# Kernel tuning notes

Measured on AMD Instinct MI355X. Metric: run time of the kernel, lower is better.

## Reference

```python
import jax, jax.numpy as jnp
import numpy as np

B, L, N, C = 4, 96, 200, 1
D, H, DH, M = 128, 8, 16, 16
DFF, E, TOPK, LAYERS = 512, 4, 2, 3
PRED, TOD = 96, 288
EPS = 1e-5


def layernorm(x, g, b):
    m = jnp.mean(x, -1, keepdims=True)
    v = jnp.mean((x - m) ** 2, -1, keepdims=True)
    return (x - m) / jnp.sqrt(v + EPS) * g + b


def performer(x, Wq, bq, Wk, bk, Wv, bv, Wo, bo, proj):
    # x: [..., S, D]; FAVOR+ softmax-kernel linear attention (non-causal)
    sh = x.shape
    def heads(t):
        return jnp.swapaxes(t.reshape(sh[:-1] + (H, DH)), -2, -3)  # [..., H, S, DH]
    q = heads(x @ Wq + bq)
    k = heads(x @ Wk + bk)
    v = heads(x @ Wv + bv)
    dn = DH ** -0.25
    q = q * dn
    k = k * dn
    qd = q @ proj  # [..., H, S, M]
    kd = k @ proj
    qn = 0.5 * jnp.sum(q * q, -1, keepdims=True)
    kn = 0.5 * jnp.sum(k * k, -1, keepdims=True)
    qp = jnp.exp(qd - qn - jnp.max(qd, -1, keepdims=True)) * (M ** -0.5) + 1e-6
    kp = jnp.exp(kd - kn - jnp.max(kd, axis=(-1, -2), keepdims=True)) * (M ** -0.5) + 1e-6
    kv = jnp.einsum('...lm,...ld->...md', kp, v)          # [..., H, M, DH]
    z = 1.0 / (jnp.einsum('...lm,...m->...l', qp, jnp.sum(kp, -2)) + 1e-6)
    o = jnp.einsum('...lm,...md->...ld', qp, kv) * z[..., None]
    o = jnp.swapaxes(o, -2, -3).reshape(sh)
    return o @ Wo + bo


def moe(x, Wg, W1, b1, W2, b2):
    # top-2 softmax gate with renormalized weights; experts are Linear-ReLU-Linear
    probs = jax.nn.softmax(x @ Wg, -1)
    tv, ti = jax.lax.top_k(probs, TOPK)
    w = tv / jnp.sum(tv, -1, keepdims=True)
    g = jnp.sum(jax.nn.one_hot(ti, E, dtype=x.dtype) * w[..., None], -2)  # [..., E]
    h = jax.nn.relu(jnp.einsum('...d,edf->...ef', x, W1) + b1)
    y = jnp.einsum('...ef,efd->...ed', h, W2) + b2
    return jnp.einsum('...ed,...e->...d', y, g)


def block(x, Wq, bq, Wk, bk, Wv, bv, Wo, bo, proj, Wg, W1, b1, W2, b2, g2, be2, g3, be3):
    a = performer(x, Wq, bq, Wk, bk, Wv, bv, Wo, bo, proj)
    x = layernorm(x + a, g2, be2)
    f = moe(x, Wg, W1, b1, W2, b2)
    return layernorm(x + f, g3, be3)


def _forward(x_enc, x_mark, emb_W, emb_b, tod_table, dow_table, adaptive_table, sp_W,
             sp_Wq, sp_bq, sp_Wk, sp_bk, sp_Wv, sp_bv, sp_Wo, sp_bo, sp_proj,
             sp_gate, sp_W1, sp_b1, sp_W2, sp_b2, sp_ln2_g, sp_ln2_b, sp_ln3_g, sp_ln3_b,
             proj_W, proj_b, LWq, Lbq, LWk, Lbk, LWv, Lbv, LWo, Lbo, Lproj,
             Lgate, LW1, Lb1, LW2, Lb2, Lln2g, Lln2b, Lln3g, Lln3b, mix_W, mix_b):
    # RevIN normalize (affine=False): stats over all dims except batch and last
    mean = jnp.mean(x_enc, axis=(1, 2), keepdims=True)
    std = jnp.sqrt(jnp.var(x_enc, axis=(1, 2), keepdims=True) + EPS)
    xn = (x_enc - mean) / std  # [B, L, N, C]
    # series decomposition, kernel=3, zero padding (count_include_pad)
    xp = jnp.pad(xn, ((0, 0), (1, 1), (0, 0), (0, 0)))
    trend = (xp[:, :-2] + xp[:, 1:-1] + xp[:, 2:]) / 3.0
    season = xn - trend
    # spatial embedding: [B,L,N,C] -> [B,N,L*C] -> [B,N,1,D] -> transformer block
    sp = jnp.swapaxes(xn, 1, 2).reshape(B, N, L * C) @ sp_W
    sp = block(sp[:, :, None, :], sp_Wq, sp_bq, sp_Wk, sp_bk, sp_Wv, sp_bv, sp_Wo, sp_bo,
               sp_proj, sp_gate, sp_W1, sp_b1, sp_W2, sp_b2, sp_ln2_g, sp_ln2_b, sp_ln3_g, sp_ln3_b)
    # trend / season embeddings with tod (col 6) and dow (col 2) mark features
    tod_f = jnp.broadcast_to(x_mark[:, :, None, 6:7], (B, L, N, 1))
    dow_f = jnp.broadcast_to(x_mark[:, :, None, 2:3], (B, L, N, 1))
    te = jnp.swapaxes(jnp.concatenate([trend, tod_f, dow_f], -1) @ emb_W + emb_b, 1, 2)  # [B,N,L,D]
    se = jnp.swapaxes(jnp.concatenate([season, tod_f, dow_f], -1) @ emb_W + emb_b, 1, 2)
    ad = jnp.broadcast_to(adaptive_table.reshape(1, N, L, D), (B, N, L, D))
    tod_idx = (x_mark[..., 6] * TOD).astype(jnp.int32)  # [B, L]
    tod_e = jnp.broadcast_to(tod_table[tod_idx][:, None], (B, N, L, D))
    dow_idx = x_mark[..., 2].astype(jnp.int32)
    dow_e = jnp.broadcast_to(dow_table[dow_idx][:, None], (B, N, L, D))
    spb = jnp.broadcast_to(sp, (B, N, L, D))
    xe = jnp.concatenate([te, se, ad, tod_e, dow_e, spb], -1) @ proj_W + proj_b  # [B,N,L,D]
    for i in range(LAYERS):
        xe = block(xe, LWq[i], Lbq[i], LWk[i], Lbk[i], LWv[i], Lbv[i], LWo[i], Lbo[i],
                   Lproj[i], Lgate[i], LW1[i], Lb1[i], LW2[i], Lb2[i],
                   Lln2g[i], Lln2b[i], Lln3g[i], Lln3b[i])
    out = xe.reshape(B, N, L * D) @ mix_W + mix_b  # [B, N, PRED*C]
    out = jnp.swapaxes(out.reshape(B, N, PRED, C), 1, 2)  # [B, PRED, N, C]
    return out * std + mean  # RevIN denorm


def setup_inputs() -> dict:
    key = jax.random.key(0)
    ks = iter(jax.random.split(key, 80))
    def nrm(shape, s=0.02):
        return jax.random.normal(next(ks), shape, jnp.float32) * s
    z = lambda shape: jnp.zeros(shape, jnp.float32)
    o = lambda shape: jnp.ones(shape, jnp.float32)
    d = {}
    d['x_enc'] = jax.random.normal(next(ks), (B, L, N, C), jnp.float32)
    xm = jax.random.uniform(next(ks), (B, L, 7), dtype=jnp.float32, minval=0.0, maxval=0.999)
    xm = xm.at[..., 2].set(jax.random.randint(next(ks), (B, L), 0, 7).astype(jnp.float32))
    d['x_mark'] = xm
    d['emb_W'] = nrm((C + 2, D)); d['emb_b'] = z((D,))
    d['tod_table'] = nrm((TOD, D)); d['dow_table'] = nrm((7, D))
    d['adaptive_table'] = nrm((L * N, D))
    d['sp_W'] = nrm((L * C, D))
    for nm in ['sp_Wq', 'sp_Wk', 'sp_Wv', 'sp_Wo']:
        d[nm] = nrm((D, D))
    for nm in ['sp_bq', 'sp_bk', 'sp_bv', 'sp_bo']:
        d[nm] = z((D,))
    d['sp_proj'] = jax.random.normal(next(ks), (DH, M), jnp.float32)
    d['sp_gate'] = nrm((D, E))
    d['sp_W1'] = nrm((E, D, DFF)); d['sp_b1'] = z((E, DFF))
    d['sp_W2'] = nrm((E, DFF, D)); d['sp_b2'] = z((E, D))
    d['sp_ln2_g'] = o((D,)); d['sp_ln2_b'] = z((D,))
    d['sp_ln3_g'] = o((D,)); d['sp_ln3_b'] = z((D,))
    d['proj_W'] = nrm((6 * D, D)); d['proj_b'] = z((D,))
    for nm in ['LWq', 'LWk', 'LWv', 'LWo']:
        d[nm] = nrm((LAYERS, D, D))
    for nm in ['Lbq', 'Lbk', 'Lbv', 'Lbo']:
        d[nm] = z((LAYERS, D))
    d['Lproj'] = jax.random.normal(next(ks), (LAYERS, DH, M), jnp.float32)
    d['Lgate'] = nrm((LAYERS, D, E))
    d['LW1'] = nrm((LAYERS, E, D, DFF)); d['Lb1'] = z((LAYERS, E, DFF))
    d['LW2'] = nrm((LAYERS, E, DFF, D)); d['Lb2'] = z((LAYERS, E, D))
    d['Lln2g'] = o((LAYERS, D)); d['Lln2b'] = z((LAYERS, D))
    d['Lln3g'] = o((LAYERS, D)); d['Lln3b'] = z((LAYERS, D))
    d['mix_W'] = nrm((L * D, PRED * C)); d['mix_b'] = z((PRED * C,))
    return d


def reference(x_enc, x_mark, emb_W, emb_b, tod_table, dow_table, adaptive_table, sp_W,
              sp_Wq, sp_bq, sp_Wk, sp_bk, sp_Wv, sp_bv, sp_Wo, sp_bo, sp_proj,
              sp_gate, sp_W1, sp_b1, sp_W2, sp_b2, sp_ln2_g, sp_ln2_b, sp_ln3_g, sp_ln3_b,
              proj_W, proj_b, LWq, Lbq, LWk, Lbk, LWv, Lbv, LWo, Lbo, Lproj,
              Lgate, LW1, Lb1, LW2, Lb2, Lln2g, Lln2b, Lln3g, Lln3b, mix_W, mix_b):
    return _forward(x_enc, x_mark, emb_W, emb_b, tod_table, dow_table, adaptive_table, sp_W,
                    sp_Wq, sp_bq, sp_Wk, sp_bk, sp_Wv, sp_bv, sp_Wo, sp_bo, sp_proj,
                    sp_gate, sp_W1, sp_b1, sp_W2, sp_b2, sp_ln2_g, sp_ln2_b, sp_ln3_g, sp_ln3_b,
                    proj_W, proj_b, LWq, Lbq, LWk, Lbk, LWv, Lbv, LWo, Lbo, Lproj,
                    Lgate, LW1, Lb1, LW2, Lb2, Lln2g, Lln2b, Lln3g, Lln3b, mix_W, mix_b)
```

## Files before the change

### kernel.cpp

```cpp
#include <hip/hip_runtime.h>
#include <stdint.h>

typedef unsigned short u16;
typedef __attribute__((ext_vector_type(8))) __bf16 bf16x8;
typedef __attribute__((ext_vector_type(4))) float f32x4;

#define Bb 4
#define Ll 96
#define Nn 200
#define Dd 128
#define Hh 8
#define Tt 76800
#define RSEQ 800
#define PREDp 96

__device__ __forceinline__ u16 f2b(float f) {
  union { float f; uint32_t u; } c; c.f = f;
  return (u16)((c.u + 0x7FFFu + ((c.u >> 16) & 1u)) >> 16);
}
__device__ __forceinline__ float b2f(u16 h) {
  union { uint32_t u; float f; } c; c.u = ((uint32_t)h) << 16;
  return c.f;
}

#define LDKV 72

template<int MODE, int DUAL, int AF32>
__global__ __launch_bounds__(256) void gemm_bf16(
    const u16* __restrict__ A, size_t aPl, const u16* __restrict__ Bt, size_t bPl,
    const float* __restrict__ bias, float* Cf, u16* Cb, size_t cPl,
    int R, int K, int N, int kchunk,
    const float* __restrict__ G, int expert, int accum)
{
  __shared__ u16 As[128 * LDKV];
  __shared__ u16 Bs[128 * LDKV];
  __shared__ u16 Asl[DUAL ? 128 * LDKV : 2];
  __shared__ u16 Bsl[DUAL ? 128 * LDKV : 2];
  const int tid = threadIdx.x;
  const int bM = blockIdx.x * 128, bN = blockIdx.y * 128;
  const int klo = blockIdx.z * kchunk;
  const int khi = (K < klo + kchunk) ? K : (klo + kchunk);
  const int wave = tid >> 6, lane = tid & 63;
  const int wr = (wave >> 1) * 64, wc = (wave & 1) * 64;
  const int lr = lane & 15, kg = (lane >> 4) * 8;
  f32x4 acc[4][4];
  const f32x4 zz = {0.f, 0.f, 0.f, 0.f};
#pragma unroll
  for (int m = 0; m < 4; m++)
#pragma unroll
    for (int n = 0; n < 4; n++) acc[m][n] = zz;

  for (int k0 = klo; k0 < khi; k0 += 64) {
#pragma unroll
    for (int i = 0; i < 4; i++) {
      int v = tid + i * 256;
      int r = v >> 3, c8 = (v & 7) * 8;
      int gr = bM + r, gc = bN + r;
      bool aok = gr < R;
      if (AF32) {
        const float* Af = (const float*)A;
        float4 f0 = make_float4(0, 0, 0, 0), f1 = make_float4(0, 0, 0, 0);
        if (aok) {
          f0 = *(const float4*)(Af + (size_t)gr * K + k0 + c8);
          f1 = *(const float4*)(Af + (size_t)gr * K + k0 + c8 + 4);
        }
        float ff[8] = {f0.x, f0.y, f0.z, f0.w, f1.x, f1.y, f1.z, f1.w};
        union { int4 v4; u16 us[8]; } hu, lu;
#pragma unroll
        for (int j = 0; j < 8; j++) {
          u16 h = f2b(ff[j]);
          hu.us[j] = h;
          lu.us[j] = f2b(ff[j] - b2f(h));
        }
        *(int4*)(&As[r * LDKV + c8]) = hu.v4;
        *(int4*)(&Asl[r * LDKV + c8]) = lu.v4;
      } else {
        int4 av = make_int4(0, 0, 0, 0);
        if (aok) av = *(const int4*)(A + (size_t)gr * K + k0 + c8);
        *(int4*)(&As[r * LDKV + c8]) = av;
        if (DUAL) {
          int4 av2 = make_int4(0, 0, 0, 0);
          if (aok) av2 = *(const int4*)(A + aPl + (size_t)gr * K + k0 + c8);
          *(int4*)(&Asl[r * LDKV + c8]) = av2;
        }
      }
      int4 bv = make_int4(0, 0, 0, 0);
      if (gc < N) bv = *(const int4*)(Bt + (size_t)gc * K + k0 + c8);
      *(int4*)(&Bs[r * LDKV + c8]) = bv;
      if (DUAL) {
        int4 bv2 = make_int4(0, 0, 0, 0);
        if (gc < N) bv2 = *(const int4*)(Bt + bPl + (size_t)gc * K + k0 + c8);
        *(int4*)(&Bsl[r * LDKV + c8]) = bv2;
      }
    }
    __syncthreads();
#pragma unroll
    for (int kk = 0; kk < 64; kk += 32) {
      bf16x8 ah[4], bh[4], al[4], bl[4];
#pragma unroll
      for (int m = 0; m < 4; m++) ah[m] = *(const bf16x8*)(&As[(wr + m * 16 + lr) * LDKV + kk + kg]);
#pragma unroll
      for (int n = 0; n < 4; n++) bh[n] = *(const bf16x8*)(&Bs[(wc + n * 16 + lr) * LDKV + kk + kg]);
      if (DUAL) {
#pragma unroll
        for (int m = 0; m < 4; m++) al[m] = *(const bf16x8*)(&Asl[(wr + m * 16 + lr) * LDKV + kk + kg]);
#pragma unroll
        for (int n = 0; n < 4; n++) bl[n] = *(const bf16x8*)(&Bsl[(wc + n * 16 + lr) * LDKV + kk + kg]);
      }
#pragma unroll
      for (int m = 0; m < 4; m++)
#pragma unroll
        for (int n = 0; n < 4; n++) {
          acc[m][n] = __builtin_amdgcn_mfma_f32_16x16x32_bf16(ah[m], bh[n], acc[m][n], 0, 0, 0);
          if (DUAL) {
            acc[m][n] = __builtin_amdgcn_mfma_f32_16x16x32_bf16(ah[m], bl[n], acc[m][n], 0, 0, 0);
            acc[m][n] = __builtin_amdgcn_mfma_f32_16x16x32_bf16(al[m], bh[n], acc[m][n], 0, 0, 0);
          }
        }
    }
    __syncthreads();
  }

  const int row0 = bM + wr + (lane >> 4) * 4;
  const int col0 = bN + wc + (lane & 15);
#pragma unroll
  for (int m = 0; m < 4; m++) {
#pragma unroll
    for (int n = 0; n < 4; n++) {
      int col = col0 + n * 16;
      if (col >= N) continue;
#pragma unroll
      for (int r = 0; r < 4; r++) {
        int row = row0 + m * 16 + r;
        if (row >= R) continue;
        float v = acc[m][n][r];
        size_t ci = (size_t)row * N + col;
        if (MODE == 3) {
          atomicAdd(Cf + ci, v);
        } else {
          if (bias) v += bias[col];
          if (MODE == 1) v = fmaxf(v, 0.f);
          if (MODE == 2) {
            v *= G[row * 4 + expert];
            if (accum) v += Cf[ci];
            Cf[ci] = v;
          } else {
            if (Cf) Cf[ci] = v;
            if (Cb) {
              u16 h = f2b(v);
              Cb[ci] = h;
              if (cPl) Cb[cPl + ci] = f2b(v - b2f(h));
            }
          }
        }
      }
    }
  }
}

#define LDH 520
__global__ __launch_bounds__(256) void moe_ffn(
    const u16* __restrict__ X2B, const u16* __restrict__ W1T, const u16* __restrict__ W2T,
    const float* __restrict__ b1, const float* __restrict__ b2,
    const float* __restrict__ G, const int* __restrict__ midx, const int* __restrict__ mcnt,
    const int* __restrict__ js, float* __restrict__ Yc)
{
  __shared__ u16 As[32 * 136];
  __shared__ u16 Ws[128 * 136];
  __shared__ u16 Hs[32 * LDH];
  __shared__ int tok_l[32];
  __shared__ int js_l[32];
  __shared__ float gt_l[32];
  const int e = blockIdx.y;
  const int cnt = mcnt[e];
  const int t0 = blockIdx.x * 32;
  if (t0 >= cnt) return;
  const int tid = threadIdx.x;
  const int wave = tid >> 6, lane = tid & 63;
  const int mw = wave >> 1, nw = wave & 1;
  const int lr = lane & 15, kg = (lane >> 4) * 8;
  const int rowq = (lane >> 4) * 4;
  if (tid < 32) {
    int slot = t0 + tid;
    int tk = (slot < cnt) ? midx[e * Tt + slot] : -1;
    tok_l[tid] = tk;
    js_l[tid] = (slot < cnt) ? js[e * Tt + slot] : 0;
    gt_l[tid] = (tk >= 0) ? G[(size_t)tk * 4 + e] : 0.f;
  }
  __syncthreads();
  {
    int v = tid;
#pragma unroll
    for (int i = 0; i < 2; i++, v += 256) {
      int r = v >> 4, c8 = (v & 15) * 8;
      int tk = tok_l[r];
      int4 av = make_int4(0, 0, 0, 0);
      if (tk >= 0) av = *(const int4*)(X2B + (size_t)tk * 128 + c8);
      *(int4*)(&As[r * 136 + c8]) = av;
    }
  }
  const u16* W1e = W1T + (size_t)e * 512 * 128;
  const u16* W2e = W2T + (size_t)e * 128 * 512;
  for (int ns = 0; ns < 4; ns++) {
    __syncthreads();
    {
      int v = tid;
#pragma unroll
      for (int i = 0; i < 8; i++, v += 256) {
        int r = v >> 4, c8 = (v & 15) * 8;
        *(int4*)(&Ws[r * 136 + c8]) = *(const int4*)(W1e + (size_t)(ns * 128 + r) * 128 + c8);
      }
    }
    __syncthreads();
    f32x4 acc[4];
    const f32x4 zz = {0.f, 0.f, 0.f, 0.f};
#pragma unroll
    for (int n = 0; n < 4; n++) acc[n] = zz;
#pragma unroll
    for (int kk = 0; kk < 128; kk += 32) {
      bf16x8 a = *(const bf16x8*)(&As[(mw * 16 + lr) * 136 + kk + kg]);
#pragma unroll
      for (int n = 0; n < 4; n++) {
        bf16x8 b = *(const bf16x8*)(&Ws[(nw * 64 + n * 16 + lr) * 136 + kk + kg]);
        acc[n] = __builtin_amdgcn_mfma_f32_16x16x32_bf16(a, b, acc[n], 0, 0, 0);
      }
    }
#pragma unroll
    for (int n = 0; n < 4; n++) {
#pragma unroll
      for (int r = 0; r < 4; r++) {
        int row = mw * 16 + rowq + r;
        int colh = ns * 128 + nw * 64 + n * 16 + lr;
        float hv = fmaxf(acc[n][r] + b1[e * 512 + colh], 0.f);
        Hs[row * LDH + (colh ^ ((row & 7) << 3))] = f2b(hv);
      }
    }
  }
  f32x4 acc2[4];
  const f32x4 zz2 = {0.f, 0.f, 0.f, 0.f};
#pragma unroll
  for (int n = 0; n < 4; n++) acc2[n] = zz2;
  for (int ks = 0; ks < 4; ks++) {
    __syncthreads();
    {
      int v = tid;
#pragma unroll
      for (int i = 0; i < 8; i++, v += 256) {
        int r = v >> 4, c8 = (v & 15) * 8;
        *(int4*)(&Ws[r * 136 + c8]) = *(const int4*)(W2e + (size_t)r * 512 + ks * 128 + c8);
      }
    }
    __syncthreads();
#pragma unroll
    for (int kk = 0; kk < 128; kk += 32) {
      int row = mw * 16 + lr;
      int k = ks * 128 + kk + kg;
      bf16x8 a = *(const bf16x8*)(&Hs[row * LDH + (k ^ ((row & 7) << 3))]);
#pragma unroll
      for (int n = 0; n < 4; n++) {
        bf16x8 b = *(const bf16x8*)(&Ws[(nw * 64 + n * 16 + lr) * 136 + kk + kg]);
        acc2[n] = __builtin_amdgcn_mfma_f32_16x16x32_bf16(a, b, acc2[n], 0, 0, 0);
      }
    }
  }
#pragma unroll
  for (int n = 0; n < 4; n++) {
#pragma unroll
    for (int r = 0; r < 4; r++) {
      int rloc = mw * 16 + rowq + r;
      if (t0 + rloc >= cnt) continue;
      int col = nw * 64 + n * 16 + lr;
      float v = (acc2[n][r] + b2[e * 128 + col]) * gt_l[rloc];
      Yc[(size_t)js_l[rloc] * 128 + col] = v;
    }
  }
}

__global__ void moe_combine(const float4* __restrict__ Yc, float4* __restrict__ Rb, int n4) {
  int i = blockIdx.x * 256 + threadIdx.x;
  if (i >= n4) return;
  int t = i >> 5, c = i & 31;
  float4 a = Yc[(size_t)t * 64 + c];
  float4 b = Yc[(size_t)t * 64 + 32 + c];
  float4 o; o.x = a.x + b.x; o.y = a.y + b.y; o.z = a.z + b.z; o.w = a.w + b.w;
  Rb[i] = o;
}

__global__ void prep_wt_tiled(const float* __restrict__ W, u16* __restrict__ Wt,
                              int K, int N, int KP, int NP, size_t PL, size_t bstride)
{
  __shared__ float tile[32][33];
  int k0 = blockIdx.x * 32, n0 = blockIdx.y * 32;
  int bb = blockIdx.z;
  const float* Wb = W + (size_t)bb * K * N;
  u16* Wtb = Wt + (size_t)bb * bstride;
  for (int i = threadIdx.y; i < 32; i += 8) {
    int k = k0 + i, n = n0 + threadIdx.x;
    tile[i][threadIdx.x] = (k < K && n < N) ? Wb[(size_t)k * N + n] : 0.f;
  }
  __syncthreads();
  for (int i = threadIdx.y; i < 32; i += 8) {
    int n = n0 + i, k = k0 + threadIdx.x;
    if (n < NP && k < KP) {
      float v = tile[threadIdx.x][i];
      u16 h = f2b(v);
      Wtb[(size_t)n * KP + k] = h;
      if (PL) Wtb[PL + (size_t)n * KP + k] = f2b(v - b2f(h));
    }
  }
}

__global__ void copy_dual(const float* __restrict__ s, u16* __restrict__ d, int n, size_t PL) {
  int i = blockIdx.x * 256 + threadIdx.x;
  if (i < n) {
    float v = s[i];
    u16 h = f2b(v);
    d[i] = h;
    d[PL + i] = f2b(v - b2f(h));
  }
}
__global__ void zero_f32(float* p, int n) {
  int i = blockIdx.x * 256 + threadIdx.x;
  if (i < n) p[i] = 0.f;
}

__global__ __launch_bounds__(256) void revin_stats(const float* __restrict__ x, float* stats) {
  int b = blockIdx.x;
  __shared__ float ss[256], sq[256];
  float s = 0.f, q = 0.f;
  for (int i = threadIdx.x; i < Ll * Nn; i += 256) {
    float v = x[(size_t)b * Ll * Nn + i];
    s += v; q += v * v;
  }
  ss[threadIdx.x] = s; sq[threadIdx.x] = q;
  __syncthreads();
  for (int st = 128; st > 0; st >>= 1) {
    if (threadIdx.x < st) { ss[threadIdx.x] += ss[threadIdx.x + st]; sq[threadIdx.x] += sq[threadIdx.x + st]; }
    __syncthreads();
  }
  if (threadIdx.x == 0) {
    float mean = ss[0] / (float)(Ll * Nn);
    float var = sq[0] / (float)(Ll * Nn) - mean * mean;
    float sd = sqrtf(var + 1e-5f);
    stats[b] = mean; stats[4 + b] = 1.f / sd; stats[8 + b] = sd;
  }
}

__global__ void calc_vecs(const float* __restrict__ embW, const float* __restrict__ embB,
                          const float* __restrict__ projW, const float* __restrict__ projB,
                          float* __restrict__ vecs)
{
  int j = threadIdx.x;
  float a = 0, b = 0, c = 0, d = 0, e = 0;
  for (int k = 0; k < 128; k++) {
    float p0 = projW[(size_t)k * 128 + j];
    float p1 = projW[(size_t)(128 + k) * 128 + j];
    a += embW[k] * p0;
    b += embW[k] * p1;
    c += embW[128 + k] * (p0 + p1);
    d += embW[256 + k] * (p0 + p1);
    e += embB[k] * (p0 + p1);
  }
  vecs[j] = a; vecs[128 + j] = b; vecs[256 + j] = c; vecs[384 + j] = d;
  vecs[512 + j] = e + projB[j];
}

__global__ void concat_qkvb(const float* __restrict__ bq, const float* __restrict__ bk,
                            const float* __restrict__ bv, float* __restrict__ out)
{
  int t = blockIdx.x * 128 + threadIdx.x;
  if (t >= 3 * 384) return;
  int layer = t / 384, r = t % 384, part = r / 128, col = r % 128;
  const float* src = part == 0 ? bq : (part == 1 ? bk : bv);
  out[t] = src[layer * 128 + col];
}

__global__ void xs_build(const float* __restrict__ x, const float* __restrict__ stats,
                         u16* __restrict__ xs, size_t PL)
{
  int r = blockIdx.x;
  int l = threadIdx.x;
  int b = r / Nn, n = r % Nn;
  float v = 0.f;
  if (l < Ll) v = (x[((size_t)(b * Ll + l) * Nn + n)] - stats[b]) * stats[4 + b];
  u16 h = f2b(v);
  xs[(size_t)r * 128 + l] = h;
  xs[PL + (size_t)r * 128 + l] = f2b(v - b2f(h));
}

__global__ __launch_bounds__(128) void sp_perf(const float* __restrict__ qf, const float* __restrict__ kf,
                                               const float* __restrict__ vf, const float* __restrict__ proj,
                                               u16* __restrict__ ob, size_t PL)
{
  int r = blockIdx.x, tid = threadIdx.x;
  __shared__ float ql[128], kl[128], vl[128], ps[256];
  ql[tid] = qf[(size_t)r * 128 + tid] * 0.5f;
  kl[tid] = kf[(size_t)r * 128 + tid] * 0.5f;
  vl[tid] = vf[(size_t)r * 128 + tid];
  ps[tid] = proj[tid]; ps[128 + tid] = proj[128 + tid];
  __syncthreads();
  int h = tid >> 4, m = tid & 15;
  float qd = 0, kd = 0, qn = 0, kn = 0;
#pragma unroll
  for (int d = 0; d < 16; d++) {
    float qv = ql[h * 16 + d], kv_ = kl[h * 16 + d];
    qd += qv * ps[d * 16 + m]; kd += kv_ * ps[d * 16 + m];
    qn += qv * qv; kn += kv_ * kv_;
  }
  qn *= 0.5f; kn *= 0.5f;
  float qmax = qd, kmax = kd;
  for (int msk = 8; msk; msk >>= 1) {
    qmax = fmaxf(qmax, __shfl_xor(qmax, msk, 16));
    kmax = fmaxf(kmax, __shfl_xor(kmax, msk, 16));
  }
  float qp = expf(qd - qn - qmax) * 0.25f + 1e-6f;
  float kp = expf(kd - kn - kmax) * 0.25f + 1e-6f;
  float t = qp * kp;
  for (int msk = 8; msk; msk >>= 1) t += __shfl_xor(t, msk, 16);
  float f = t / (t + 1e-6f);
  float o = vl[tid] * f;
  u16 hh = f2b(o);
  ob[(size_t)r * 128 + tid] = hh;
  ob[PL + (size_t)r * 128 + tid] = f2b(o - b2f(hh));
}

__global__ __launch_bounds__(256) void performer_attn2(
    const float* __restrict__ qkv, const float* __restrict__ proj, float* __restrict__ ao)
{
  __shared__ float ks[2][96 * 17];
  __shared__ float vs[2][96 * 17];
  __shared__ float kvs[2][16 * 17];
  __shared__ float ksum[2][16];
  __shared__ float red[2][96];
  __shared__ float ps[256];
  const int tid = threadIdx.x;
  const int seq = blockIdx.x >> 2, hp = blockIdx.x & 3;
  ps[tid] = proj[tid];
#pragma unroll
  for (int i = 0; i < 3; i++) {
    int idx = tid + i * 256;
    int row = idx >> 3, c4 = idx & 7;
    int hl = c4 >> 2, d0 = (c4 & 3) * 4;
    size_t gb = ((size_t)seq * 96 + row) * 384 + hp * 32 + hl * 16 + d0;
    float4 k4 = *(const float4*)(qkv + gb + 128);
    float4 v4 = *(const float4*)(qkv + gb + 256);
    int lb = row * 17 + d0;
    ks[hl][lb + 0] = k4.x * 0.5f; ks[hl][lb + 1] = k4.y * 0.5f;
    ks[hl][lb + 2] = k4.z * 0.5f; ks[hl][lb + 3] = k4.w * 0.5f;
    vs[hl][lb + 0] = v4.x; vs[hl][lb + 1] = v4.y;
    vs[hl][lb + 2] = v4.z; vs[hl][lb + 3] = v4.w;
  }
  const int h = tid / 96, s = tid - h * 96;
  float q[16];
  if (tid < 192) {
    size_t qb_ = ((size_t)seq * 96 + s) * 384 + hp * 32 + h * 16;
#pragma unroll
    for (int i = 0; i < 4; i++) {
      float4 t = *(const float4*)(qkv + qb_ + i * 4);
      q[i * 4] = t.x * 0.5f; q[i * 4 + 1] = t.y * 0.5f;
      q[i * 4 + 2] = t.z * 0.5f; q[i * 4 + 3] = t.w * 0.5f;
    }
  }
  __syncthreads();
  float qd[16], kd[16], qp[16];
  float qn = 0.f, kn = 0.f;
  if (tid < 192) {
#pragma unroll
    for (int d = 0; d < 16; d++) {
      float kv = ks[h][s * 17 + d];
      qn += q[d] * q[d]; kn += kv * kv;
    }
    qn *= 0.5f; kn *= 0.5f;
#pragma unroll
    for (int m = 0; m < 16; m++) {
      float aq = 0.f, ak = 0.f;
#pragma unroll
      for (int d = 0; d < 16; d++) {
        aq += q[d] * ps[d * 16 + m];
        ak += ks[h][s * 17 + d] * ps[d * 16 + m];
      }
      qd[m] = aq; kd[m] = ak;
    }
    float km = kd[0];
#pragma unroll
    for (int m = 1; m < 16; m++) km = fmaxf(km, kd[m]);
    red[h][s] = km;
  }
  __syncthreads();
  if (tid < 192 && s < 48) red[h][s] = fmaxf(red[h][s], red[h][s + 48]);
  __syncthreads();
  if (tid < 192 && s < 24) red[h][s] = fmaxf(red[h][s], red[h][s + 24]);
  __syncthreads();
  if (tid < 192 && s < 12) red[h][s] = fmaxf(red[h][s], red[h][s + 12]);
  __syncthreads();
  if (tid < 192 && s < 6) red[h][s] = fmaxf(red[h][s], red[h][s + 6]);
  __syncthreads();
  if (tid < 192 && s < 3) red[h][s] = fmaxf(red[h][s], red[h][s + 3]);
  __syncthreads();
  if (tid < 192) {
    float kmax = fmaxf(fmaxf(red[h][0], red[h][1]), red[h][2]);
    float qmx = qd[0];
#pragma unroll
    for (int m = 1; m < 16; m++) qmx = fmaxf(qmx, qd[m]);
#pragma unroll
    for (int m = 0; m < 16; m++) {
      qp[m] = expf(qd[m] - qn - qmx) * 0.25f + 1e-6f;
      ks[h][s * 17 + m] = expf(kd[m] - kn - kmax) * 0.25f + 1e-6f;
    }
  }
  __syncthreads();
#pragma unroll
  for (int it = 0; it < 2; it++) {
    int idx = tid + it * 256;
    int hh = idx >> 8, mm = (idx >> 4) & 15, dd = idx & 15;
    float a0 = 0.f, a1 = 0.f, a2 = 0.f, a3 = 0.f;
    for (int s2 = 0; s2 < 96; s2 += 4) {
      a0 += ks[hh][(s2 + 0) * 17 + mm] * vs[hh][(s2 + 0) * 17 + dd];
      a1 += ks[hh][(s2 + 1) * 17 + mm] * vs[hh][(s2 + 1) * 17 + dd];
      a2 += ks[hh][(s2 + 2) * 17 + mm] * vs[hh][(s2 + 2) * 17 + dd];
      a3 += ks[hh][(s2 + 3) * 17 + mm] * vs[hh][(s2 + 3) * 17 + dd];
    }
    kvs[hh][mm * 17 + dd] = (a0 + a1) + (a2 + a3);
  }
  if (tid < 32) {
    int hh = tid >> 4, mm = tid & 15;
    float a0 = 0.f, a1 = 0.f, a2 = 0.f, a3 = 0.f;
    for (int s2 = 0; s2 < 96; s2 += 4) {
      a0 += ks[hh][(s2 + 0) * 17 + mm];
      a1 += ks[hh][(s2 + 1) * 17 + mm];
      a2 += ks[hh][(s2 + 2) * 17 + mm];
      a3 += ks[hh][(s2 + 3) * 17 + mm];
    }
    ksum[hh][mm] = (a0 + a1) + (a2 + a3);
  }
  __syncthreads();
  if (tid < 192) {
    float zd = 1e-6f;
#pragma unroll
    for (int m = 0; m < 16; m++) zd += qp[m] * ksum[h][m];
    float zi = 1.f / zd;
#pragma unroll
    for (int d = 0; d < 16; d++) {
      float a = 0.f;
#pragma unroll
      for (int m = 0; m < 16; m++) a += qp[m] * kvs[h][m * 17 + d];
      ks[h][s * 17 + d] = a * zi;
    }
  }
  __syncthreads();
#pragma unroll
  for (int i = 0; i < 3; i++) {
    int idx = tid + i * 256;
    int row = idx >> 3, c4 = idx & 7;
    int hl = c4 >> 2, d0 = (c4 & 3) * 4;
    int lb = row * 17 + d0;
    float4 o;
    o.x = ks[hl][lb + 0]; o.y = ks[hl][lb + 1]; o.z = ks[hl][lb + 2]; o.w = ks[hl][lb + 3];
    *(float4*)(ao + ((size_t)seq * 96 + row) * 128 + hp * 32 + hl * 16 + d0) = o;
  }
}

__global__ __launch_bounds__(256) void ln_fused(const u16* __restrict__ Xin, size_t xPl,
    const float* __restrict__ Res,
    const float* __restrict__ g, const float* __restrict__ bta,
    u16* __restrict__ Out, size_t oPl, int R)
{
  int wave = threadIdx.x >> 6, lane = threadIdx.x & 63;
  int tok = blockIdx.x * 4 + wave;
  if (tok >= R) return;
  size_t bo = (size_t)tok * 128 + lane * 2;
  ushort2 h2 = *(const ushort2*)(Xin + bo);
  ushort2 l2 = *(const ushort2*)(Xin + xPl + bo);
  float2 rv = *(const float2*)(Res + bo);
  float a0 = b2f(h2.x) + b2f(l2.x) + rv.x;
  float a1 = b2f(h2.y) + b2f(l2.y) + rv.y;
  float s = a0 + a1, sq = a0 * a0 + a1 * a1;
  for (int m = 32; m; m >>= 1) { s += __shfl_xor(s, m); sq += __shfl_xor(sq, m); }
  float mean = s * (1.f / 128.f);
  float var = sq * (1.f / 128.f) - mean * mean;
  float rstd = rsqrtf(var + 1e-5f);
  float g0 = g[lane * 2], g1 = g[lane * 2 + 1], b0 = bta[lane * 2], b1 = bta[lane * 2 + 1];
  float o0 = (a0 - mean) * rstd * g0 + b0;
  float o1 = (a1 - mean) * rstd * g1 + b1;
  u16 u0 = f2b(o0), u1 = f2b(o1);
  ushort2 hh; hh.x = u0; hh.y = u1;
  ushort2 ll; ll.x = f2b(o0 - b2f(u0)); ll.y = f2b(o1 - b2f(u1));
  *(ushort2*)(Out + bo) = hh;
  *(ushort2*)(Out + oPl + bo) = ll;
}

__global__ __launch_bounds__(256) void gate_topk(const u16* __restrict__ X, size_t xPl,
    const float* __restrict__ Wg, float* __restrict__ Gout, int R)
{
  int gid = blockIdx.x * 256 + threadIdx.x;
  int tok = gid >> 2, sub = gid & 3;
  if (tok >= R) return;
  float pr0 = 0, pr1 = 0, pr2 = 0, pr3 = 0;
  for (int d0 = 0; d0 < 32; d0 += 8) {
    size_t idx = (size_t)tok * 128 + sub * 32 + d0;
    int4 hv = *(const int4*)(X + idx);
    int4 lv = *(const int4*)(X + xPl + idx);
    const u16* hp = (const u16*)&hv;
    const u16* lp = (const u16*)&lv;
#pragma unroll
    for (int j = 0; j < 8; j++) {
      float xj = b2f(hp[j]) + b2f(lp[j]);
      float4 w = *(const float4*)(Wg + (size_t)(sub * 32 + d0 + j) * 4);
      pr0 += xj * w.x; pr1 += xj * w.y; pr2 += xj * w.z; pr3 += xj * w.w;
    }
  }
  pr0 += __shfl_xor(pr0, 1, 4); pr0 += __shfl_xor(pr0, 2, 4);
  pr1 += __shfl_xor(pr1, 1, 4); pr1 += __shfl_xor(pr1, 2, 4);
  pr2 += __shfl_xor(pr2, 1, 4); pr2 += __shfl_xor(pr2, 2, 4);
  pr3 += __shfl_xor(pr3, 1, 4); pr3 += __shfl_xor(pr3, 2, 4);
  float mx = fmaxf(fmaxf(pr0, pr1), fmaxf(pr2, pr3));
  float e0 = expf(pr0 - mx), e1 = expf(pr1 - mx), e2 = expf(pr2 - mx), e3 = expf(pr3 - mx);
  int i1 = 0; float t1 = e0;
  if (e1 > t1) { t1 = e1; i1 = 1; }
  if (e2 > t1) { t1 = e2; i1 = 2; }
  if (e3 > t1) { t1 = e3; i1 = 3; }
  float t2 = -1.f; int i2 = 0;
  if (0 != i1 && e0 > t2) { t2 = e0; i2 = 0; }
  if (1 != i1 && e1 > t2) { t2 = e1; i2 = 1; }
  if (2 != i1 && e2 > t2) { t2 = e2; i2 = 2; }
  if (3 != i1 && e3 > t2) { t2 = e3; i2 = 3; }
  float own = (sub == 0) ? e0 : ((sub == 1) ? e1 : ((sub == 2) ? e2 : e3));
  float gv = (sub == i1 || sub == i2) ? own / (t1 + t2) : 0.f;
  Gout[(size_t)tok * 4 + sub] = gv;
}

__global__ void moe_zero_counts(int* counts) {
  if (threadIdx.x < 4) counts[threadIdx.x] = 0;
}
__global__ __launch_bounds__(256) void moe_fill(const float* __restrict__ G,
    int* __restrict__ counts, int* __restrict__ idx, int* __restrict__ js, int R)
{
  int tok = blockIdx.x * 256 + threadIdx.x;
  if (tok >= R) return;
  float4 g = *(const float4*)(G + (size_t)tok * 4);
  int j = 0;
  if (g.x > 0.f) { int p = atomicAdd(counts + 0, 1); idx[0 * Tt + p] = tok; js[0 * Tt + p] = tok * 2 + j; j++; }
  if (g.y > 0.f) { int p = atomicAdd(counts + 1, 1); idx[1 * Tt + p] = tok; js[1 * Tt + p] = tok * 2 + j; j++; }
  if (g.z > 0.f) { int p = atomicAdd(counts + 2, 1); idx[2 * Tt + p] = tok; js[2 * Tt + p] = tok * 2 + j; j++; }
  if (g.w > 0.f) { int p = atomicAdd(counts + 3, 1); idx[3 * Tt + p] = tok; js[3 * Tt + p] = tok * 2 + j; j++; }
}

__global__ __launch_bounds__(128) void embed_combine(
    const float* __restrict__ xenc, const float* __restrict__ xmark,
    const float* __restrict__ stats, const float* __restrict__ vecs,
    const float* __restrict__ adP, const float* __restrict__ ttP,
    const float* __restrict__ ddP, const float* __restrict__ spP,
    u16* __restrict__ XB, size_t PL)
{
  int t = blockIdx.x;
  int l = t % 96; int bn = t / 96; int n = bn % Nn; int b = bn / Nn;
  float mean = stats[b], rstd = stats[4 + b];
  float x0 = (xenc[((size_t)(b * Ll + l) * Nn + n)] - mean) * rstd;
  float xm = 0.f, xp = 0.f;
  if (l > 0)  xm = (xenc[((size_t)(b * Ll + l - 1) * Nn + n)] - mean) * rstd;
  if (l < 95) xp = (xenc[((size_t)(b * Ll + l + 1) * Nn + n)] - mean) * rstd;
  float trend = (xm + x0 + xp) * (1.f / 3.f);
  float season = x0 - trend;
  const float* mk = xmark + (size_t)(b * Ll + l) * 7;
  float todf = mk[6], dowf = mk[2];
  int ti = (int)(todf * 288.f);
  int di = (int)dowf;
  int j = threadIdx.x;
  float v = trend * vecs[j] + season * vecs[128 + j] + todf * vecs[256 + j] + dowf * vecs[384 + j]
          + vecs[512 + j]
          + adP[((size_t)n * 96 + l) * 128 + j]
          + ttP[(size_t)ti * 128 + j]
          + ddP[(size_t)di * 128 + j]
          + spP[(size_t)bn * 128 + j];
  u16 h = f2b(v);
  XB[(size_t)t * 128 + j] = h;
  XB[PL + (size_t)t * 128 + j] = f2b(v - b2f(h));
}

__global__ void final_out(const float* __restrict__ mixC, const float* __restrict__ mixb,
                          const float* __restrict__ stats, float* __restrict__ out)
{
  int i = blockIdx.x * 256 + threadIdx.x;
  if (i >= Bb * PREDp * Nn) return;
  int n = i % Nn; int p = (i / Nn) % PREDp; int b = i / (Nn * PREDp);
  out[i] = (mixC[((size_t)(b * Nn + n)) * PREDp + p] + mixb[p]) * stats[8 + b] + stats[b];
}

extern "C" void kernel_launch(void* const* d_in, const int* in_sizes, int n_in,
                              void* d_out, int out_size, void* d_ws, size_t ws_size,
                              hipStream_t stream)
{
  const float* x_enc   = (const float*)d_in[0];
  const float* x_mark  = (const float*)d_in[1];
  const float* emb_W   = (const float*)d_in[2];
  const float* emb_b   = (const float*)d_in[3];
  const float* tod_tab = (const float*)d_in[4];
  const float* dow_tab = (const float*)d_in[5];
  const float* adapt   = (const float*)d_in[6];
  const float* sp_W    = (const float*)d_in[7];
  const float* sp_Wq   = (const float*)d_in[8];
  const float* sp_Wk   = (const float*)d_in[9];
  const float* sp_Wv   = (const float*)d_in[10];
  const float* sp_Wo   = (const float*)d_in[11];
  const float* sp_bq   = (const float*)d_in[12];
  const float* sp_bk   = (const float*)d_in[13];
  const float* sp_bv   = (const float*)d_in[14];
  const float* sp_bo   = (const float*)d_in[15];
  const float* sp_proj = (const float*)d_in[16];
  const float* sp_gate = (const float*)d_in[17];
  const float* sp_W1   = (const float*)d_in[18];
  const float* sp_b1   = (const float*)d_in[19];
  const float* sp_W2   = (const float*)d_in[20];
  const float* sp_b2   = (const float*)d_in[21];
  const float* sp_l2g  = (const float*)d_in[22];
  const float* sp_l2b  = (const float*)d_in[23];
  const float* sp_l3g  = (const float*)d_in[24];
  const float* sp_l3b  = (const float*)d_in[25];
  const float* proj_W  = (const float*)d_in[26];
  const float* proj_b  = (const float*)d_in[27];
  const float* LWq     = (const float*)d_in[28];
  const float* LWk     = (const float*)d_in[29];
  const float* LWv     = (const float*)d_in[30];
  const float* LWo     = (const float*)d_in[31];
  const float* Lbq     = (const float*)d_in[32];
  const float* Lbk     = (const float*)d_in[33];
  const float* Lbv     = (const float*)d_in[34];
  const float* Lbo     = (const float*)d_in[35];
  const float* Lproj   = (const float*)d_in[36];
  const float* Lgate   = (const float*)d_in[37];
  const float* LW1     = (const float*)d_in[38];
  const float* Lb1     = (const float*)d_in[39];
  const float* LW2     = (const float*)d_in[40];
  const float* Lb2     = (const float*)d_in[41];
  const float* Ll2g    = (const float*)d_in[42];
  const float* Ll2b    = (const float*)d_in[43];
  const float* Ll3g    = (const float*)d_in[44];
  const float* Ll3b    = (const float*)d_in[45];
  const float* mix_W   = (const float*)d_in[46];
  const float* mix_b   = (const float*)d_in[47];

  if (n_in < 48) return;
  if (in_sizes[0] != Bb * Ll * Nn) return;
  if (in_sizes[26] != 768 * 128) return;
  if (in_sizes[38] != 3 * 4 * 128 * 512) return;
  if (in_sizes[46] != 12288 * 96) return;

  char* base = (char*)d_ws;
  size_t off = 0;
  auto alloc = [&](size_t bytes) -> char* {
    char* p = base + off;
    off += (bytes + 255) & ~(size_t)255;
    return p;
  };
  const size_t PT128 = (size_t)Tt * 128;
  const int CH = Tt / 2;

  float* stats = (float*)alloc(12 * 4);
  float* vecs  = (float*)alloc(5 * 128 * 4);
  float* mixC  = (float*)alloc((size_t)RSEQ * 96 * 4);
  float* Gt    = (float*)alloc((size_t)Tt * 4 * 4);
  float* Gsp   = (float*)alloc((size_t)RSEQ * 4 * 4);
  int* midx    = (int*)alloc((size_t)4 * Tt * 4);
  int* jsarr   = (int*)alloc((size_t)4 * Tt * 4);
  int* mcnt    = (int*)alloc(256);
  float* qkvb  = (float*)alloc((size_t)3 * 384 * 4);
  u16* XB    = (u16*)alloc(PT128 * 2 * 2);
  u16* X2B   = (u16*)alloc(PT128 * 2 * 2);
  float* Rb  = (float*)alloc(PT128 * 4);
  u16* spWt  = (u16*)alloc((size_t)128 * 128 * 2 * 2);
  u16* spWqT = (u16*)alloc((size_t)128 * 128 * 2 * 2);
  u16* spWkT = (u16*)alloc((size_t)128 * 128 * 2 * 2);
  u16* spWvT = (u16*)alloc((size_t)128 * 128 * 2 * 2);
  u16* spWoT = (u16*)alloc((size_t)128 * 128 * 2 * 2);
  u16* LWqkvT = (u16*)alloc((size_t)3 * 384 * 128 * 2 * 2);
  u16* LWoT  = (u16*)alloc((size_t)3 * 128 * 128 * 2 * 2);
  u16* spW1T = (u16*)alloc((size_t)4 * 512 * 128 * 2 * 2);
  u16* spW2T = (u16*)alloc((size_t)4 * 128 * 512 * 2 * 2);
  u16* LW1T  = (u16*)alloc((size_t)12 * 512 * 128 * 2);
  u16* LW2T  = (u16*)alloc((size_t)12 * 128 * 512 * 2);
  u16* PT    = (u16*)alloc((size_t)4 * 128 * 128 * 2 * 2);
  u16* mixWT = (u16*)alloc((size_t)96 * 12288 * 2 * 2);

  const size_t B3 = (size_t)Tt * 2 * 128 * 4;
  char* regB = alloc(B3);
  size_t boff = 0;
  auto balloc = [&](size_t bytes) -> char* {
    char* p = regB + boff;
    boff += (bytes + 255) & ~(size_t)255;
    return p;
  };
  float* adP   = (float*)balloc((size_t)19200 * 128 * 4);
  float* ttP   = (float*)balloc((size_t)288 * 128 * 4);
  float* ddP   = (float*)balloc((size_t)7 * 128 * 4);
  float* spP   = (float*)balloc((size_t)RSEQ * 128 * 4);
  u16* adb     = (u16*)balloc((size_t)19200 * 128 * 2 * 2);
  u16* ttb     = (u16*)balloc((size_t)288 * 128 * 2 * 2);
  u16* ddb     = (u16*)balloc((size_t)7 * 128 * 2 * 2);
  const size_t SPL = (size_t)RSEQ * 128;
  u16* xsb     = (u16*)balloc(SPL * 2 * 2);
  u16* sp0b    = (u16*)balloc(SPL * 2 * 2);
  u16* spaob   = (u16*)balloc(SPL * 2 * 2);
  u16* spx2b   = (u16*)balloc(SPL * 2 * 2);
  u16* spob    = (u16*)balloc(SPL * 2 * 2);
  u16* Hsp     = (u16*)balloc((size_t)RSEQ * 512 * 2 * 2);
  float* spq   = (float*)balloc(SPL * 4);
  float* spk   = (float*)balloc(SPL * 4);
  float* spv   = (float*)balloc(SPL * 4);
  float* spR   = (float*)balloc(SPL * 4);
  float* QKVf = (float*)regB;
  float* AOf  = QKVf + (size_t)CH * 384;
  float* Yc = (float*)regB;
  if (off > ws_size || boff > B3) return;

  const size_t PL_PT = (size_t)4 * 128 * 128;
  const size_t QKVPL = (size_t)3 * 384 * 128;
  const size_t WOPL  = (size_t)3 * 128 * 128;
  u16* P2T = PT;
  u16* P3T = PT + 128 * 128;
  u16* P4T = PT + 2 * 128 * 128;
  u16* P5T = PT + 3 * 128 * 128;

  auto tp = [&](const float* W, u16* Wt, int K, int N, int KP, int NP, int nb,
                size_t PL, size_t bstride) {
    dim3 g((KP + 31) / 32, (NP + 31) / 32, nb);
    prep_wt_tiled<<<g, dim3(32, 8), 0, stream>>>(W, Wt, K, N, KP, NP, PL, bstride);
  };
  auto gd = [&](const u16* A, size_t aPl, const u16* Bt, size_t bPl, const float* bias,
                float* Cf, u16* Cb, size_t cPl, int R, int K, int N) {
    dim3 g((R + 127) / 128, (N + 127) / 128, 1);
    gemm_bf16<0, 1, 0><<<g, 256, 0, stream>>>(A, aPl, Bt, bPl, bias, Cf, Cb, cPl,
        R, K, N, K, nullptr, 0, 0);
  };
  auto cpb = [&](const float* s, u16* d, int n, size_t PL) {
    copy_dual<<<(n + 255) / 256, 256, 0, stream>>>(s, d, n, PL);
  };

  revin_stats<<<4, 256, 0, stream>>>(x_enc, stats);
  tp(sp_W, spWt, 96, 128, 128, 128, 1, 128 * 128, 128 * 128);
  tp(sp_Wq, spWqT, 128, 128, 128, 128, 1, 128 * 128, 128 * 128);
  tp(sp_Wk, spWkT, 128, 128, 128, 128, 1, 128 * 128, 128 * 128);
  tp(sp_Wv, spWvT, 128, 128, 128, 128, 1, 128 * 128, 128 * 128);
  tp(sp_Wo, spWoT, 128, 128, 128, 128, 1, 128 * 128, 128 * 128);
  tp(LWq, LWqkvT + 0 * 128 * 128, 128, 128, 128, 128, 3, QKVPL, (size_t)384 * 128);
  tp(LWk, LWqkvT + 1 * 128 * 128, 128, 128, 128, 128, 3, QKVPL, (size_t)384 * 128);
  tp(LWv, LWqkvT + 2 * 128 * 128, 128, 128, 128, 128, 3, QKVPL, (size_t)384 * 128);
  tp(LWo, LWoT, 128, 128, 128, 128, 3, WOPL, (size_t)128 * 128);
  tp(sp_W1, spW1T, 128, 512, 128, 512, 4, (size_t)4 * 512 * 128, (size_t)512 * 128);
  tp(sp_W2, spW2T, 512, 128, 512, 128, 4, (size_t)4 * 128 * 512, (size_t)128 * 512);
  tp(LW1, LW1T, 128, 512, 128, 512, 12, 0, (size_t)512 * 128);
  tp(LW2, LW2T, 512, 128, 512, 128, 12, 0, (size_t)128 * 512);
  tp(proj_W + 256 * 128, PT, 128, 128, 128, 128, 4, PL_PT, (size_t)128 * 128);
  tp(mix_W, mixWT, 12288, 96, 12288, 96, 1, (size_t)96 * 12288, (size_t)96 * 12288);
  cpb(adapt, adb, 19200 * 128, (size_t)19200 * 128);
  cpb(tod_tab, ttb, 288 * 128, (size_t)288 * 128);
  cpb(dow_tab, ddb, 7 * 128, (size_t)7 * 128);
  calc_vecs<<<1, 128, 0, stream>>>(emb_W, emb_b, proj_W, proj_b, vecs);
  concat_qkvb<<<(3 * 384 + 127) / 128, 128, 0, stream>>>(Lbq, Lbk, Lbv, qkvb);

  gd(adb, (size_t)19200 * 128, P2T, PL_PT, nullptr, adP, nullptr, 0, 19200, 128, 128);
  gd(ttb, (size_t)288 * 128, P3T, PL_PT, nullptr, ttP, nullptr, 0, 288, 128, 128);
  gd(ddb, (size_t)7 * 128, P4T, PL_PT, nullptr, ddP, nullptr, 0, 7, 128, 128);

  xs_build<<<RSEQ, 128, 0, stream>>>(x_enc, stats, xsb, SPL);
  gd(xsb, SPL, spWt, 128 * 128, nullptr, nullptr, sp0b, SPL, RSEQ, 128, 128);
  gd(sp0b, SPL, spWqT, 128 * 128, sp_bq, spq, nullptr, 0, RSEQ, 128, 128);
  gd(sp0b, SPL, spWkT, 128 * 128, sp_bk, spk, nullptr, 0, RSEQ, 128, 128);
  gd(sp0b, SPL, spWvT, 128 * 128, sp_bv, spv, nullptr, 0, RSEQ, 128, 128);
  sp_perf<<<RSEQ, 128, 0, stream>>>(spq, spk, spv, sp_proj, spaob, SPL);
  gd(spaob, SPL, spWoT, 128 * 128, sp_bo, spR, nullptr, 0, RSEQ, 128, 128);
  ln_fused<<<RSEQ / 4, 256, 0, stream>>>(sp0b, SPL, spR, sp_l2g, sp_l2b, spx2b, SPL, RSEQ);
  gate_topk<<<(RSEQ * 4 + 255) / 256, 256, 0, stream>>>(spx2b, SPL, sp_gate, Gsp, RSEQ);
  for (int e = 0; e < 4; e++) {
    dim3 g1g((RSEQ + 127) / 128, 4, 1);
    gemm_bf16<1, 1, 0><<<g1g, 256, 0, stream>>>(spx2b, SPL, spW1T + (size_t)e * 512 * 128,
        (size_t)4 * 512 * 128, sp_b1 + e * 512, nullptr, Hsp, (size_t)RSEQ * 512,
        RSEQ, 128, 512, 128, nullptr, 0, 0);
    dim3 g2g((RSEQ + 127) / 128, 1, 1);
    gemm_bf16<2, 1, 0><<<g2g, 256, 0, stream>>>(Hsp, (size_t)RSEQ * 512,
        spW2T + (size_t)e * 128 * 512, (size_t)4 * 128 * 512, sp_b2 + e * 128, spR, nullptr, 0,
        RSEQ, 512, 128, 512, Gsp, e, e > 0);
  }
  ln_fused<<<RSEQ / 4, 256, 0, stream>>>(spx2b, SPL, spR, sp_l3g, sp_l3b, spob, SPL, RSEQ);
  gd(spob, SPL, P5T, PL_PT, nullptr, spP, nullptr, 0, RSEQ, 128, 128);

  embed_combine<<<Tt, 128, 0, stream>>>(x_enc, x_mark, stats, vecs, adP, ttP, ddP, spP, XB, PT128);

  for (int i = 0; i < 3; i++) {
    for (int c = 0; c < 2; c++) {
      const u16* XBc = XB + (size_t)c * CH * 128;
      {
        dim3 g((CH + 127) / 128, 3, 1);
        gemm_bf16<0, 1, 0><<<g, 256, 0, stream>>>(XBc, PT128, LWqkvT + (size_t)i * 384 * 128,
            QKVPL, qkvb + i * 384, QKVf, nullptr, 0, CH, 128, 384, 128, nullptr, 0, 0);
      }
      performer_attn2<<<(RSEQ / 2) * 4, 256, 0, stream>>>(QKVf, Lproj + i * 256, AOf);
      {
        dim3 g((CH + 127) / 128, 1, 1);
        gemm_bf16<0, 1, 1><<<g, 256, 0, stream>>>((const u16*)AOf, 0,
            LWoT + (size_t)i * 128 * 128, WOPL, Lbo + i * 128, Rb + (size_t)c * CH * 128,
            nullptr, 0, CH, 128, 128, 128, nullptr, 0, 0);
      }
    }
    ln_fused<<<Tt / 4, 256, 0, stream>>>(XB, PT128, Rb, Ll2g + i * 128, Ll2b + i * 128, X2B, PT128, Tt);
    gate_topk<<<(Tt * 4 + 255) / 256, 256, 0, stream>>>(X2B, PT128, Lgate + i * 512, Gt, Tt);
    moe_zero_counts<<<1, 64, 0, stream>>>(mcnt);
    moe_fill<<<(Tt + 255) / 256, 256, 0, stream>>>(Gt, mcnt, midx, jsarr, Tt);
    moe_ffn<<<dim3((Tt + 31) / 32, 4), 256, 0, stream>>>(
        X2B, LW1T + (size_t)i * 4 * 512 * 128, LW2T + (size_t)i * 4 * 128 * 512,
        Lb1 + i * 4 * 512, Lb2 + i * 4 * 128, Gt, midx, mcnt, jsarr, Yc);
    moe_combine<<<(Tt * 32 + 255) / 256, 256, 0, stream>>>((const float4*)Yc, (float4*)Rb, Tt * 32);
    ln_fused<<<Tt / 4, 256, 0, stream>>>(X2B, PT128, Rb, Ll3g + i * 128, Ll3b + i * 128, XB, PT128, Tt);
  }

  zero_f32<<<(RSEQ * 96 + 255) / 256, 256, 0, stream>>>(mixC, RSEQ * 96);
  {
    dim3 g((RSEQ + 127) / 128, 1, 16);
    gemm_bf16<3, 1, 0><<<g, 256, 0, stream>>>(XB, PT128, mixWT, (size_t)96 * 12288, nullptr,
        mixC, nullptr, 0, RSEQ, 12288, 96, 768, nullptr, 0, 0);
  }
  final_out<<<(Bb * PREDp * Nn + 255) / 256, 256, 0, stream>>>(mixC, mix_b, stats, (float*)d_out);
}
```

Measured before the change: 2.278 ms.

## Retile MoE FFN to 64-token tiles, interleave W1/W2 chunks, fuse combine into LayerNorm

The MoE expert kernel now processes 64 tokens per block, with each wave owning 16 rows and all 128 columns. It also interleaves the two expert GEMMs per 128-wide hidden chunk, so the hidden activations only need a 64x136 buffer instead of the full 512-wide row. The separate moe_combine kernel is removed, and the layernorm now reads both top-2 expert outputs directly through a second residual pointer with a stride. Together these cut kernel launches and a full pass over the expert output buffer, and they raise per-block MFMA reuse of weight tiles, at the cost of more accumulator registers per thread.

```diff
diff --git a/kernel.cpp b/kernel.cpp
--- a/kernel.cpp
+++ b/kernel.cpp
@@ -158,29 +158,28 @@
   }
 }
 
-#define LDH 520
+#define MT 64
 __global__ __launch_bounds__(256) void moe_ffn(
     const u16* __restrict__ X2B, const u16* __restrict__ W1T, const u16* __restrict__ W2T,
     const float* __restrict__ b1, const float* __restrict__ b2,
     const float* __restrict__ G, const int* __restrict__ midx, const int* __restrict__ mcnt,
     const int* __restrict__ js, float* __restrict__ Yc)
 {
-  __shared__ u16 As[32 * 136];
+  __shared__ u16 As[MT * 136];
   __shared__ u16 Ws[128 * 136];
-  __shared__ u16 Hs[32 * LDH];
-  __shared__ int tok_l[32];
-  __shared__ int js_l[32];
-  __shared__ float gt_l[32];
+  __shared__ u16 Hs[MT * 136];
+  __shared__ int tok_l[MT];
+  __shared__ int js_l[MT];
+  __shared__ float gt_l[MT];
   const int e = blockIdx.y;
   const int cnt = mcnt[e];
-  const int t0 = blockIdx.x * 32;
+  const int t0 = blockIdx.x * MT;
   if (t0 >= cnt) return;
   const int tid = threadIdx.x;
   const int wave = tid >> 6, lane = tid & 63;
-  const int mw = wave >> 1, nw = wave & 1;
   const int lr = lane & 15, kg = (lane >> 4) * 8;
   const int rowq = (lane >> 4) * 4;
-  if (tid < 32) {
+  if (tid < MT) {
     int slot = t0 + tid;
     int tk = (slot < cnt) ? midx[e * Tt + slot] : -1;
     tok_l[tid] = tk;
@@ -191,7 +190,7 @@
   {
     int v = tid;
 #pragma unroll
-    for (int i = 0; i < 2; i++, v += 256) {
+    for (int i = 0; i < 4; i++, v += 256) {
       int r = v >> 4, c8 = (v & 15) * 8;
       int tk = tok_l[r];
       int4 av = make_int4(0, 0, 0, 0);
@@ -201,6 +200,11 @@
   }
   const u16* W1e = W1T + (size_t)e * 512 * 128;
   const u16* W2e = W2T + (size_t)e * 128 * 512;
+  f32x4 acc2[8];
+  const f32x4 zz = {0.f, 0.f, 0.f, 0.f};
+#pragma unroll
+  for (int n = 0; n < 8; n++) acc2[n] = zz;
+
   for (int ns = 0; ns < 4; ns++) {
     __syncthreads();
     {
@@ -212,78 +216,59 @@
       }
     }
     __syncthreads();
-    f32x4 acc[4];
-    const f32x4 zz = {0.f, 0.f, 0.f, 0.f};
-#pragma unroll
-    for (int n = 0; n < 4; n++) acc[n] = zz;
+    f32x4 acc1[8];
+#pragma unroll
+    for (int n = 0; n < 8; n++) acc1[n] = zz;
 #pragma unroll
     for (int kk = 0; kk < 128; kk += 32) {
-      bf16x8 a = *(const bf16x8*)(&As[(mw * 16 + lr) * 136 + kk + kg]);
-#pragma unroll
-      for (int n = 0; n < 4; n++) {
-        bf16x8 b = *(const bf16x8*)(&Ws[(nw * 64 + n * 16 + lr) * 136 + kk + kg]);
-        acc[n] = __builtin_amdgcn_mfma_f32_16x16x32_bf16(a, b, acc[n], 0, 0, 0);
-      }
-    }
-#pragma unroll
-    for (int n = 0; n < 4; n++) {
+      bf16x8 a = *(const bf16x8*)(&As[(wave * 16 + lr) * 136 + kk + kg]);
+#pragma unroll
+      for (int n = 0; n < 8; n++) {
+        bf16x8 b = *(const bf16x8*)(&Ws[(n * 16 + lr) * 136 + kk + kg]);
+        acc1[n] = __builtin_amdgcn_mfma_f32_16x16x32_bf16(a, b, acc1[n], 0, 0, 0);
+      }
+    }
+#pragma unroll
+    for (int n = 0; n < 8; n++) {
 #pragma unroll
       for (int r = 0; r < 4; r++) {
-        int row = mw * 16 + rowq + r;
-        int colh = ns * 128 + nw * 64 + n * 16 + lr;
-        float hv = fmaxf(acc[n][r] + b1[e * 512 + colh], 0.f);
-        Hs[row * LDH + (colh ^ ((row & 7) << 3))] = f2b(hv);
-      }
-    }
-  }
-  f32x4 acc2[4];
-  const f32x4 zz2 = {0.f, 0.f, 0.f, 0.f};
-#pragma unroll
-  for (int n = 0; n < 4; n++) acc2[n] = zz2;
-  for (int ks = 0; ks < 4; ks++) {
+        int row = wave * 16 + rowq + r;
+        int col = n * 16 + lr;
+        float hv = fmaxf(acc1[n][r] + b1[e * 512 + ns * 128 + col], 0.f);
+        Hs[row * 136 + col] = f2b(hv);
+      }
+    }
     __syncthreads();
     {
       int v = tid;
 #pragma unroll
       for (int i = 0; i < 8; i++, v += 256) {
         int r = v >> 4, c8 = (v & 15) * 8;
-        *(int4*)(&Ws[r * 136 + c8]) = *(const int4*)(W2e + (size_t)r * 512 + ks * 128 + c8);
+        *(int4*)(&Ws[r * 136 + c8]) = *(const int4*)(W2e + (size_t)r * 512 + ns * 128 + c8);
       }
     }
     __syncthreads();
 #pragma unroll
     for (int kk = 0; kk < 128; kk += 32) {
-      int row = mw * 16 + lr;
-      int k = ks * 128 + kk + kg;
-      bf16x8 a = *(const bf16x8*)(&Hs[row * LDH + (k ^ ((row & 7) << 3))]);
-#pragma unroll
-      for (int n = 0; n < 4; n++) {
-        bf16x8 b = *(const bf16x8*)(&Ws[(nw * 64 + n * 16 + lr) * 136 + kk + kg]);
-        acc2[n] = __builtin_amdgcn_mfma_f32_16x16x32_bf16(a, b, acc2[n], 0, 0, 0);
-      }
-    }
-  }
-#pragma unroll
-  for (int n = 0; n < 4; n++) {
+      bf16x8 a2 = *(const bf16x8*)(&Hs[(wave * 16 + lr) * 136 + kk + kg]);
+#pragma unroll
+      for (int n = 0; n < 8; n++) {
+        bf16x8 b2v = *(const bf16x8*)(&Ws[(n * 16 + lr) * 136 + kk + kg]);
+        acc2[n] = __builtin_amdgcn_mfma_f32_16x16x32_bf16(a2, b2v, acc2[n], 0, 0, 0);
+      }
+    }
+  }
+#pragma unroll
+  for (int n = 0; n < 8; n++) {
 #pragma unroll
     for (int r = 0; r < 4; r++) {
-      int rloc = mw * 16 + rowq + r;
-      if (t0 + rloc >= cnt) continue;
-      int col = nw * 64 + n * 16 + lr;
-      float v = (acc2[n][r] + b2[e * 128 + col]) * gt_l[rloc];
-      Yc[(size_t)js_l[rloc] * 128 + col] = v;
-    }
-  }
-}
-
-__global__ void moe_combine(const float4* __restrict__ Yc, float4* __restrict__ Rb, int n4) {
-  int i = blockIdx.x * 256 + threadIdx.x;
-  if (i >= n4) return;
-  int t = i >> 5, c = i & 31;
-  float4 a = Yc[(size_t)t * 64 + c];
-  float4 b = Yc[(size_t)t * 64 + 32 + c];
-  float4 o; o.x = a.x + b.x; o.y = a.y + b.y; o.z = a.z + b.z; o.w = a.w + b.w;
-  Rb[i] = o;
+      int row = wave * 16 + rowq + r;
+      if (t0 + row >= cnt) continue;
+      int col = n * 16 + lr;
+      float v = (acc2[n][r] + b2[e * 128 + col]) * gt_l[row];
+      Yc[(size_t)js_l[row] * 128 + col] = v;
+    }
+  }
 }
 
 __global__ void prep_wt_tiled(const float* __restrict__ W, u16* __restrict__ Wt,
@@ -561,7 +546,7 @@
 }
 
 __global__ __launch_bounds__(256) void ln_fused(const u16* __restrict__ Xin, size_t xPl,
-    const float* __restrict__ Res,
+    const float* __restrict__ Res, int rStride, const float* __restrict__ Res2,
     const float* __restrict__ g, const float* __restrict__ bta,
     u16* __restrict__ Out, size_t oPl, int R)
 {
@@ -569,11 +554,16 @@
   int tok = blockIdx.x * 4 + wave;
   if (tok >= R) return;
   size_t bo = (size_t)tok * 128 + lane * 2;
+  size_t ro = (size_t)tok * rStride + lane * 2;
   ushort2 h2 = *(const ushort2*)(Xin + bo);
   ushort2 l2 = *(const ushort2*)(Xin + xPl + bo);
-  float2 rv = *(const float2*)(Res + bo);
+  float2 rv = *(const float2*)(Res + ro);
   float a0 = b2f(h2.x) + b2f(l2.x) + rv.x;
   float a1 = b2f(h2.y) + b2f(l2.y) + rv.y;
+  if (Res2) {
+    float2 r2 = *(const float2*)(Res2 + ro);
+    a0 += r2.x; a1 += r2.y;
+  }
   float s = a0 + a1, sq = a0 * a0 + a1 * a1;
   for (int m = 32; m; m >>= 1) { s += __shfl_xor(s, m); sq += __shfl_xor(sq, m); }
   float mean = s * (1.f / 128.f);
@@ -868,7 +858,7 @@
   gd(sp0b, SPL, spWvT, 128 * 128, sp_bv, spv, nullptr, 0, RSEQ, 128, 128);
   sp_perf<<<RSEQ, 128, 0, stream>>>(spq, spk, spv, sp_proj, spaob, SPL);
   gd(spaob, SPL, spWoT, 128 * 128, sp_bo, spR, nullptr, 0, RSEQ, 128, 128);
-  ln_fused<<<RSEQ / 4, 256, 0, stream>>>(sp0b, SPL, spR, sp_l2g, sp_l2b, spx2b, SPL, RSEQ);
+  ln_fused<<<RSEQ / 4, 256, 0, stream>>>(sp0b, SPL, spR, 128, nullptr, sp_l2g, sp_l2b, spx2b, SPL, RSEQ);
   gate_topk<<<(RSEQ * 4 + 255) / 256, 256, 0, stream>>>(spx2b, SPL, sp_gate, Gsp, RSEQ);
   for (int e = 0; e < 4; e++) {
     dim3 g1g((RSEQ + 127) / 128, 4, 1);
@@ -880,7 +870,7 @@
         spW2T + (size_t)e * 128 * 512, (size_t)4 * 128 * 512, sp_b2 + e * 128, spR, nullptr, 0,
         RSEQ, 512, 128, 512, Gsp, e, e > 0);
   }
-  ln_fused<<<RSEQ / 4, 256, 0, stream>>>(spx2b, SPL, spR, sp_l3g, sp_l3b, spob, SPL, RSEQ);
+  ln_fused<<<RSEQ / 4, 256, 0, stream>>>(spx2b, SPL, spR, 128, nullptr, sp_l3g, sp_l3b, spob, SPL, RSEQ);
   gd(spob, SPL, P5T, PL_PT, nullptr, spP, nullptr, 0, RSEQ, 128, 128);
 
   embed_combine<<<Tt, 128, 0, stream>>>(x_enc, x_mark, stats, vecs, adP, ttP, ddP, spP, XB, PT128);
@@ -901,15 +891,16 @@
             nullptr, 0, CH, 128, 128, 128, nullptr, 0, 0);
       }
     }
-    ln_fused<<<Tt / 4, 256, 0, stream>>>(XB, PT128, Rb, Ll2g + i * 128, Ll2b + i * 128, X2B, PT128, Tt);
+    ln_fused<<<Tt / 4, 256, 0, stream>>>(XB, PT128, Rb, 128, nullptr,
+                                         Ll2g + i * 128, Ll2b + i * 128, X2B, PT128, Tt);
     gate_topk<<<(Tt * 4 + 255) / 256, 256, 0, stream>>>(X2B, PT128, Lgate + i * 512, Gt, Tt);
     moe_zero_counts<<<1, 64, 0, stream>>>(mcnt);
     moe_fill<<<(Tt + 255) / 256, 256, 0, stream>>>(Gt, mcnt, midx, jsarr, Tt);
-    moe_ffn<<<dim3((Tt + 31) / 32, 4), 256, 0, stream>>>(
+    moe_ffn<<<dim3((Tt + MT - 1) / MT, 4), 256, 0, stream>>>(
         X2B, LW1T + (size_t)i * 4 * 512 * 128, LW2T + (size_t)i * 4 * 128 * 512,
         Lb1 + i * 4 * 512, Lb2 + i * 4 * 128, Gt, midx, mcnt, jsarr, Yc);
-    moe_combine<<<(Tt * 32 + 255) / 256, 256, 0, stream>>>((const float4*)Yc, (float4*)Rb, Tt * 32);
-    ln_fused<<<Tt / 4, 256, 0, stream>>>(X2B, PT128, Rb, Ll3g + i * 128, Ll3b + i * 128, XB, PT128, Tt);
+    ln_fused<<<Tt / 4, 256, 0, stream>>>(X2B, PT128, Yc, 256, Yc + 128,
+                                         Ll3g + i * 128, Ll3b + i * 128, XB, PT128, Tt);
   }
 
   zero_f32<<<(RSEQ * 96 + 255) / 256, 256, 0, stream>>>(mixC, RSEQ * 96);
```

Result: faster. 2.178 ms (-4.4%).
